# Kernel tuning notes

Measured on AMD Instinct MI355X. Metric: run time of the kernel, lower is better.

The kernel has to match this reference:

```python
import jax, jax.numpy as jnp
import numpy as np

EPS = 1e-5

def _layer_norm(x, gamma, beta):
    # LayerNorm over the last two dims [C, 128], matching nn.LayerNorm([C, 128])
    mean = jnp.mean(x, axis=(-2, -1), keepdims=True)
    var = jnp.var(x, axis=(-2, -1), keepdims=True)
    return (x - mean) * jax.lax.rsqrt(var + EPS) * gamma + beta


def setup_inputs() -> dict:
    key = jax.random.key(0)
    ks = jax.random.split(key, 7)
    B, C, N, L = 64, 1024, 128, 512
    W_SCALE = 0.02  # keep pre-softmax logits / activations in a sane range
    return {
        "X_in": jax.random.normal(ks[0], (B, C, N), jnp.float32),
        "T": jax.random.normal(ks[1], (B, C, L), jnp.float32),
        "Wq": jax.random.normal(ks[2], (C, C), jnp.float32) * W_SCALE,
        "Wk": jax.random.normal(ks[3], (C, C), jnp.float32) * W_SCALE,
        "Wv": jax.random.normal(ks[4], (C, C), jnp.float32) * W_SCALE,
        "Wf1": jax.random.normal(ks[5], (C, C), jnp.float32) * W_SCALE,
        "Wf2": jax.random.normal(ks[6], (C, C), jnp.float32) * W_SCALE,
        "gamma": jnp.ones((C, N), jnp.float32),
        "beta": jnp.zeros((C, N), jnp.float32),
    }


def reference(X_in, T, Wq, Wk, Wv, Wf1, Wf2, gamma, beta):
    C = Wq.shape[1]  # feature_map_cs (intended value of the buggy X_in.weight.shape[1])
    # 1x1 Conv1d == per-position channel matmul: weight [out, in]
    q = jnp.einsum('oc,bcn->bon', Wq, X_in)      # [B, C, N]
    k = jnp.einsum('oc,bcl->bol', Wk, T)         # [B, C, L]
    sim = jnp.einsum('bcn,bcl->bnl', q, k) / jnp.sqrt(jnp.float32(C))  # [B, N, L]
    attn = jax.nn.softmax(sim, axis=2)           # softmax over tokens L
    v = jnp.einsum('oc,bcl->bol', Wv, T)         # [B, C, L]
    ctx = jnp.einsum('bcl,bnl->bcn', v, attn)    # [B, C, N] == bmm(values, attn^T)
    X_out = _layer_norm(X_in + ctx, gamma, beta)
    h = jax.nn.relu(jnp.einsum('oc,bcn->bon', Wf1, X_out))
    ffn = jnp.einsum('oc,bcn->bon', Wf2, h)
    return _layer_norm(X_out + ffn, gamma, beta)
```

## Files before the change

### kernel.cpp

```cpp
#include <hip/hip_runtime.h>


using bf16   = __bf16;
using bf16x4 = __attribute__((ext_vector_type(4))) __bf16;
using bf16x8 = __attribute__((ext_vector_type(8))) __bf16;
using f32x4  = __attribute__((ext_vector_type(4))) float;

static constexpr int  Bb = 64;
static constexpr int  Cc = 1024;
static constexpr int  Nn = 128;
static constexpr int  Ll = 512;
static constexpr long long PLANE = (long long)Cc * Nn;
static constexpr float INV_PLANE = 1.0f / 131072.0f;

__device__ __forceinline__ void gload_lds16(const void* g, void* l) {
    __builtin_amdgcn_global_load_lds(
        (__attribute__((address_space(1))) void*)g,
        (__attribute__((address_space(3))) void*)l,
        16, 0, 0);
}

__global__ void __launch_bounds__(256)
prep_all(const float* __restrict__ Wv, const float* __restrict__ Wf1,
         const float* __restrict__ Wf2, const float* __restrict__ Wq,
         const float* __restrict__ Wk, const float* __restrict__ X,
         bf16* __restrict__ WvB, bf16* __restrict__ Wf1B, bf16* __restrict__ Wf2B,
         bf16* __restrict__ WqT, bf16* __restrict__ WkT, bf16* __restrict__ Xt) {
    __shared__ float tile[64][65];
    const int bx = blockIdx.x;
    const int t  = threadIdx.x;
    if (bx < 3072) {
        const float* in = bx < 1024 ? Wv : (bx < 2048 ? Wf1 : Wf2);
        bf16* out       = bx < 1024 ? WvB : (bx < 2048 ? Wf1B : Wf2B);
        int i = (bx & 1023) * 256 + t;
        float4 v = reinterpret_cast<const float4*>(in)[i];
        bf16x4 o = { (bf16)v.x, (bf16)v.y, (bf16)v.z, (bf16)v.w };
        reinterpret_cast<bf16x4*>(out)[i] = o;
        return;
    }
    const float* in; bf16* outT;
    int R, S, bxx, byy, bz = 0;
    if (bx < 3584) {
        int j = bx - 3072;
        in = (j >= 256) ? Wk : Wq; outT = (j >= 256) ? WkT : WqT;
        R = Cc; S = Cc; j &= 255; bxx = j & 15; byy = j >> 4;
    } else {
        int j = bx - 3584; bz = j >> 5; j &= 31;
        bxx = j & 1; byy = j >> 1; in = X; outT = Xt; R = Cc; S = Nn;
    }
    long long plane = (long long)R * S;
    in   += (long long)bz * plane;
    outT += (long long)bz * plane;
    int s0 = bxx * 64, r0 = byy * 64;
    int rl = t >> 4, sc = (t & 15) * 4;
    #pragma unroll
    for (int p = 0; p < 4; ++p) {
        int r = p * 16 + rl;
        float4 v = *(const float4*)(in + (long long)(r0 + r) * S + s0 + sc);
        *(float4*)&tile[r][sc] = v;
    }
    __syncthreads();
    long long tb = ((long long)(s0 >> 6) * (R >> 6) + (r0 >> 6)) * 4096;
    int sb = t >> 3, rg = (t & 7) * 8;
    #pragma unroll
    for (int p = 0; p < 2; ++p) {
        int s = sb + p * 32;
        bf16x8 o;
        #pragma unroll
        for (int j = 0; j < 8; ++j) o[j] = (bf16)tile[rg + j][s];
        *(bf16x8*)(outT + tb + s * 64 + rg) = o;
    }
}

#define GEMM_PROLOGUE_AND_LOOP(A_, Bt_, KLOOP_, LD_, TA_, TB_)                     \
    __shared__ bf16 As[2][128 * 64];                                               \
    __shared__ bf16 Bs[2][128 * 64];                                               \
    const int n0   = blockIdx.x * 128;                                             \
    const int m0   = blockIdx.y * 128;                                             \
    const int t    = threadIdx.x;                                                  \
    const int lane = t & 63;                                                       \
    const int w    = t >> 6;                                                       \
    const int wr   = (w >> 1) * 64;                                                \
    const int wc   = (w & 1) * 64;                                                 \
    const int lr   = lane & 15;                                                    \
    const int hi4  = (lane >> 4) * 16;                                             \
    const int sw   = (lr & 7) << 4;                                                \
    const int stepA_ = (TA_) ? 4096 : 64;                                          \
    const int stepB_ = (TB_) ? 4096 : 64;                                          \
    const bf16* gA[4]; const bf16* gB[4]; int lo[4];                               \
    _Pragma("unroll")                                                              \
    for (int p = 0; p < 4; ++p) {                                                  \
        int o = w * 1024 + lane * 16 + p * 4096;                                   \
        int row = o >> 7;                                                          \
        int scol = ((o & 127) ^ ((row & 7) << 4)) >> 1;                            \
        lo[p] = o;                                                                 \
        int ra = m0 + row, rb = n0 + row;                                          \
        gA[p] = (TA_) ? A_ + ((long long)(ra >> 6) * (LD_ >> 6)) * 4096            \
                           + (ra & 63) * 64 + scol                                 \
                      : A_ + (long long)ra * LD_ + scol;                           \
        gB[p] = (TB_) ? Bt_ + ((long long)(rb >> 6) * (LD_ >> 6)) * 4096           \
                            + (rb & 63) * 64 + scol                                \
                      : Bt_ + (long long)rb * LD_ + scol;                          \
    }                                                                              \
    f32x4 acc[4][4] = {};                                                          \
    const int NT_ = KLOOP_ / 64;                                                   \
    _Pragma("unroll")                                                              \
    for (int p = 0; p < 4; ++p) gload_lds16(gA[p], (char*)As[0] + lo[p]);          \
    _Pragma("unroll")                                                              \
    for (int p = 0; p < 4; ++p) gload_lds16(gB[p], (char*)Bs[0] + lo[p]);          \
    __syncthreads();                                                               \
    int cur_ = 0;                                                                  \
    for (int kt = 0; kt < NT_; ++kt) {                                             \
        if (kt + 1 < NT_) {                                                        \
            _Pragma("unroll")                                                      \
            for (int p = 0; p < 4; ++p)                                            \
                gload_lds16(gA[p] + (long long)(kt + 1) * stepA_,                  \
                            (char*)As[cur_ ^ 1] + lo[p]);                          \
            _Pragma("unroll")                                                      \
            for (int p = 0; p < 4; ++p)                                            \
                gload_lds16(gB[p] + (long long)(kt + 1) * stepB_,                  \
                            (char*)Bs[cur_ ^ 1] + lo[p]);                          \
        }                                                                          \
        const bf16* As_ = As[cur_]; const bf16* Bs_ = Bs[cur_];                    \
        _Pragma("unroll")                                                          \
        for (int kk = 0; kk < 2; ++kk) {                                           \
            bf16x8 af[4], bfr[4];                                                  \
            _Pragma("unroll")                                                      \
            for (int i = 0; i < 4; ++i) {                                          \
                int ra = wr + i * 16 + lr;                                         \
                int rb = wc + i * 16 + lr;                                         \
                af[i]  = *(const bf16x8*)((const char*)As_ +                       \
                          ((((ra << 7) + (kk << 6) + hi4)) ^ sw));                 \
                bfr[i] = *(const bf16x8*)((const char*)Bs_ +                       \
                          ((((rb << 7) + (kk << 6) + hi4)) ^ sw));                 \
            }                                                                      \
            _Pragma("unroll")                                                      \
            for (int mi = 0; mi < 4; ++mi)                                         \
                _Pragma("unroll")                                                  \
                for (int ni = 0; ni < 4; ++ni)                                     \
                    acc[mi][ni] = __builtin_amdgcn_mfma_f32_16x16x32_bf16(         \
                        af[mi], bfr[ni], acc[mi][ni], 0, 0, 0);                    \
        }                                                                          \
        __syncthreads();                                                           \
        cur_ ^= 1;                                                                 \
    }

template <typename OutT, bool RELU, int TA, int TB>
__global__ void __launch_bounds__(256, 2)
gemm_tn(const bf16* __restrict__ A, const bf16* __restrict__ Bt, OutT* __restrict__ C,
        int M, int N, int KLOOP, int ld, long long sA, long long sBt, long long sC,
        float scale) {
    A  += (long long)blockIdx.z * sA;
    Bt += (long long)blockIdx.z * sBt;
    C  += (long long)blockIdx.z * sC;
    GEMM_PROLOGUE_AND_LOOP(A, Bt, KLOOP, ld, TA, TB)
    const int rbase = m0 + wr + (lane >> 4) * 4;
    const int cbase = n0 + wc + lr;
    #pragma unroll
    for (int mi = 0; mi < 4; ++mi)
        #pragma unroll
        for (int ni = 0; ni < 4; ++ni)
            #pragma unroll
            for (int r = 0; r < 4; ++r) {
                float v = acc[mi][ni][r] * scale;
                if (RELU) v = fmaxf(v, 0.0f);
                C[(long long)(rbase + mi * 16 + r) * N + (cbase + ni * 16)] = (OutT)v;
            }
}

__global__ void g2_reduce(const float* __restrict__ p, bf16* __restrict__ g2) {
    int i = (blockIdx.x * 256 + threadIdx.x) * 4;
    float4 a = *(const float4*)(p + i);
    float4 b = *(const float4*)(p + 1048576 + i);
    float4 c = *(const float4*)(p + 2097152 + i);
    float4 d = *(const float4*)(p + 3145728 + i);
    bf16x4 o = { (bf16)(a.x + b.x + c.x + d.x), (bf16)(a.y + b.y + c.y + d.y),
                 (bf16)(a.z + b.z + c.z + d.z), (bf16)(a.w + b.w + c.w + d.w) };
    *(bf16x4*)(g2 + i) = o;
}

__global__ void __launch_bounds__(256, 3)
gemm_sim_exp(const bf16* __restrict__ A , const float* __restrict__ Tg,
             bf16* __restrict__ E, float* __restrict__ rspart) {
    __shared__ char smem[50432];
    bf16*  Asb = (bf16*)smem;
    bf16*  Bs  = (bf16*)(smem + 16384);
    bf16*  scr = (bf16*)(smem + 32768);
    float* rs  = (float*)(smem + 49408);
    A  += (long long)blockIdx.z * ((long long)Nn * Cc);
    Tg += (long long)blockIdx.z * ((long long)Cc * Ll);
    E  += (long long)blockIdx.z * ((long long)Nn * Ll);
    const int n0 = blockIdx.x * 128;
    const int t = threadIdx.x, lane = t & 63, w = t >> 6;
    const int wr = (w >> 1) * 64, wc = (w & 1) * 64;
    const int lr = lane & 15, hi4 = (lane >> 4) * 16, sw = (lr & 7) << 4;
    const bf16* gA[4]; int lo[4];
    #pragma unroll
    for (int p = 0; p < 4; ++p) {
        int o = w * 1024 + lane * 16 + p * 4096;
        int row = o >> 7;
        int scol = ((o & 127) ^ ((row & 7) << 4)) >> 1;
        lo[p] = o;
        gA[p] = A + (long long)row * Cc + scol;
    }
    const int s1_rc = t >> 2, s1_l = (t & 3) * 32;
    const int s2_l = t & 127, s2_ch = (t >> 7) * 8;
    float4 treg[8];
    #pragma unroll
    for (int i = 0; i < 8; ++i)
        treg[i] = *(const float4*)(Tg + (long long)s1_rc * Ll + n0 + s1_l + i * 4);
    f32x4 acc[4][4] = {};
    const int NT = Cc / 64;
    for (int kt = 0; kt < NT; ++kt) {
        #pragma unroll
        for (int i = 0; i < 8; ++i) {
            float4 v = treg[i];
            bf16x4 o = { (bf16)v.x, (bf16)v.y, (bf16)v.z, (bf16)v.w };
            *(bf16x4*)(scr + s1_rc * 130 + s1_l + i * 4) = o;
        }
        __syncthreads();
        #pragma unroll
        for (int p = 0; p < 4; ++p) gload_lds16(gA[p] + kt * 64, (char*)Asb + lo[p]);
        #pragma unroll
        for (int g = 0; g < 4; ++g) {
            int c0 = s2_ch + g * 16;
            bf16x8 bv;
            #pragma unroll
            for (int j = 0; j < 8; ++j) bv[j] = scr[(c0 + j) * 130 + s2_l];
            *(bf16x8*)((char*)Bs + ((s2_l * 128 + c0 * 2) ^ ((s2_l & 7) << 4))) = bv;
        }
        if (kt + 1 < NT) {
            #pragma unroll
            for (int i = 0; i < 8; ++i)
                treg[i] = *(const float4*)(Tg + (long long)((kt + 1) * 64 + s1_rc) * Ll
                                           + n0 + s1_l + i * 4);
        }
        __syncthreads();
        #pragma unroll
        for (int kk = 0; kk < 2; ++kk) {
            bf16x8 af[4], bfr[4];
            #pragma unroll
            for (int i = 0; i < 4; ++i) {
                int ra = wr + i * 16 + lr;
                int rb = wc + i * 16 + lr;
                af[i]  = *(const bf16x8*)((const char*)Asb + (((ra << 7) + (kk << 6) + hi4) ^ sw));
                bfr[i] = *(const bf16x8*)((const char*)Bs  + (((rb << 7) + (kk << 6) + hi4) ^ sw));
            }
            #pragma unroll
            for (int mi = 0; mi < 4; ++mi)
                #pragma unroll
                for (int ni = 0; ni < 4; ++ni)
                    acc[mi][ni] = __builtin_amdgcn_mfma_f32_16x16x32_bf16(
                        af[mi], bfr[ni], acc[mi][ni], 0, 0, 0);
        }
    }
    const int rbase = wr + (lane >> 4) * 4;
    const int cbase = n0 + wc + lr;
    float psum[4][4];
    #pragma unroll
    for (int mi = 0; mi < 4; ++mi)
        #pragma unroll
        for (int r = 0; r < 4; ++r) psum[mi][r] = 0.f;
    #pragma unroll
    for (int mi = 0; mi < 4; ++mi)
        #pragma unroll
        for (int ni = 0; ni < 4; ++ni)
            #pragma unroll
            for (int r = 0; r < 4; ++r) {
                float ev = __expf(acc[mi][ni][r] * 0.03125f);
                E[(long long)(rbase + mi * 16 + r) * Ll + (cbase + ni * 16)] = (bf16)ev;
                psum[mi][r] += ev;
            }
    #pragma unroll
    for (int mi = 0; mi < 4; ++mi)
        #pragma unroll
        for (int r = 0; r < 4; ++r) {
            float v = psum[mi][r];
            v += __shfl_xor(v, 1); v += __shfl_xor(v, 2);
            v += __shfl_xor(v, 4); v += __shfl_xor(v, 8);
            psum[mi][r] = v;
        }
    __syncthreads();
    if (lr == 0) {
        #pragma unroll
        for (int mi = 0; mi < 4; ++mi)
            #pragma unroll
            for (int r = 0; r < 4; ++r)
                rs[(wc ? 1 : 0) * 128 + wr + (lane >> 4) * 4 + mi * 16 + r] = psum[mi][r];
    }
    __syncthreads();
    if (t < 128)
        rspart[((long long)blockIdx.z * 4 + blockIdx.x) * 128 + t] = rs[t] + rs[128 + t];
}

__global__ void __launch_bounds__(256, 2)
gemm_u_scaled(const bf16* __restrict__ A , const float* __restrict__ Tg,
              bf16* __restrict__ C, const float* __restrict__ rspart) {
    __shared__ char smem[49152];
    bf16* AsB = (bf16*)smem;
    bf16* Bs  = (bf16*)(smem + 32768);
    A  += (long long)blockIdx.z * ((long long)Nn * Ll);
    Tg += (long long)blockIdx.z * ((long long)Cc * Ll);
    C  += (long long)blockIdx.z * ((long long)Nn * Cc);
    const float* rp = rspart + (long long)blockIdx.z * 512;
    const int n0 = blockIdx.x * 128;
    const int t = threadIdx.x, lane = t & 63, w = t >> 6;
    const int wr = (w >> 1) * 64, wc = (w & 1) * 64;
    const int lr = lane & 15, hi4 = (lane >> 4) * 16, sw = (lr & 7) << 4;
    const bf16* gA[4]; int lo[4];
    #pragma unroll
    for (int p = 0; p < 4; ++p) {
        int o = w * 1024 + lane * 16 + p * 4096;
        int row = o >> 7;
        int scol = ((o & 127) ^ ((row & 7) << 4)) >> 1;
        lo[p] = o;
        gA[p] = A + (long long)row * Ll + scol;
    }
    const int s_c = t >> 1, s_half = (t & 1) * 32;
    float4 treg[8];
    #pragma unroll
    for (int p = 0; p < 4; ++p) gload_lds16(gA[p], (char*)AsB + lo[p]);
    #pragma unroll
    for (int i = 0; i < 8; ++i)
        treg[i] = *(const float4*)(Tg + (long long)(n0 + s_c) * Ll + s_half + i * 4);
    f32x4 acc[4][4] = {};
    int cur = 0;
    const int NT = Ll / 64;
    for (int kt = 0; kt < NT; ++kt) {
        if (kt + 1 < NT) {
            #pragma unroll
            for (int p = 0; p < 4; ++p)
                gload_lds16(gA[p] + (kt + 1) * 64, (char*)AsB + (cur ^ 1) * 16384 + lo[p]);
        }
        __syncthreads();
        #pragma unroll
        for (int q = 0; q < 4; ++q) {
            bf16x8 bv;
            #pragma unroll
            for (int j = 0; j < 4; ++j) {
                bv[j]     = (bf16)((const float*)&treg[q * 2])[j];
                bv[4 + j] = (bf16)((const float*)&treg[q * 2 + 1])[j];
            }
            *(bf16x8*)((char*)Bs + ((s_c * 128 + (s_half + q * 8) * 2) ^ ((s_c & 7) << 4))) = bv;
        }
        if (kt + 1 < NT) {
            #pragma unroll
            for (int i = 0; i < 8; ++i)
                treg[i] = *(const float4*)(Tg + (long long)(n0 + s_c) * Ll
                                           + (kt + 1) * 64 + s_half + i * 4);
        }
        __syncthreads();
        const bf16* As_ = AsB + cur * 8192;
        #pragma unroll
        for (int kk = 0; kk < 2; ++kk) {
            bf16x8 af[4], bfr[4];
            #pragma unroll
            for (int i = 0; i < 4; ++i) {
                int ra = wr + i * 16 + lr;
                int rb = wc + i * 16 + lr;
                af[i]  = *(const bf16x8*)((const char*)As_ + (((ra << 7) + (kk << 6) + hi4) ^ sw));
                bfr[i] = *(const bf16x8*)((const char*)Bs  + (((rb << 7) + (kk << 6) + hi4) ^ sw));
            }
            #pragma unroll
            for (int mi = 0; mi < 4; ++mi)
                #pragma unroll
                for (int ni = 0; ni < 4; ++ni)
                    acc[mi][ni] = __builtin_amdgcn_mfma_f32_16x16x32_bf16(
                        af[mi], bfr[ni], acc[mi][ni], 0, 0, 0);
        }
        cur ^= 1;
    }
    const int rbase = wr + (lane >> 4) * 4;
    const int cbase = n0 + wc + lr;
    #pragma unroll
    for (int mi = 0; mi < 4; ++mi)
        #pragma unroll
        for (int r = 0; r < 4; ++r) {
            int row = rbase + mi * 16 + r;
            float inv = 1.f / (rp[row] + rp[128 + row] + rp[256 + row] + rp[384 + row]);
            #pragma unroll
            for (int ni = 0; ni < 4; ++ni)
                C[(long long)row * Cc + (cbase + ni * 16)] = (bf16)(acc[mi][ni][r] * inv);
        }
}

__global__ void __launch_bounds__(256, 2)
gemm_ctx_ln1(const bf16* __restrict__ A , const bf16* __restrict__ Bt ,
             const float* __restrict__ X, bf16* __restrict__ Z1, float* __restrict__ partials,
             int K, long long sBt) {
    const int N = Nn;
    Bt += (long long)blockIdx.z * sBt;
    X  += (long long)blockIdx.z * PLANE;
    Z1 += (long long)blockIdx.z * PLANE;
    GEMM_PROLOGUE_AND_LOOP(A, Bt, K, K, 0, 0)
    const int rbase = m0 + wr + (lane >> 4) * 4;
    const int cbase = n0 + wc + lr;
    float s = 0.f, ss = 0.f;
    #pragma unroll
    for (int mi = 0; mi < 4; ++mi)
        #pragma unroll
        for (int ni = 0; ni < 4; ++ni)
            #pragma unroll
            for (int r = 0; r < 4; ++r) {
                long long idx = (long long)(rbase + mi * 16 + r) * N + (cbase + ni * 16);
                float zv = acc[mi][ni][r] + X[idx];
                Z1[idx] = (bf16)zv;
                s += zv; ss += zv * zv;
            }
    #pragma unroll
    for (int off = 32; off; off >>= 1) { s += __shfl_xor(s, off); ss += __shfl_xor(ss, off); }
    __shared__ float red[8];
    if (lane == 0) { red[w] = s; red[4 + w] = ss; }
    __syncthreads();
    if (t == 0) {
        float S = red[0] + red[1] + red[2] + red[3];
        float SS = red[4] + red[5] + red[6] + red[7];
        float* p = partials + ((long long)blockIdx.z * 8 + blockIdx.y) * 2;
        p[0] = S; p[1] = SS;
    }
}

__global__ void __launch_bounds__(256, 2)
gemm_ffn_ln2(const bf16* __restrict__ A , const bf16* __restrict__ Bt ,
             const bf16* __restrict__ Z1, const float* __restrict__ pp1,
             const float* __restrict__ gamma, const float* __restrict__ beta,
             bf16* __restrict__ Z2, float* __restrict__ partials,
             int K, long long sA) {
    A  += (long long)blockIdx.z * sA;
    Z1 += (long long)blockIdx.z * PLANE;
    Z2 += (long long)blockIdx.z * PLANE;
    float S1 = 0.f, SS1 = 0.f;
    #pragma unroll
    for (int j = 0; j < 8; ++j) {
        S1  += pp1[((long long)blockIdx.z * 8 + j) * 2];
        SS1 += pp1[((long long)blockIdx.z * 8 + j) * 2 + 1];
    }
    const float mean1 = S1 * INV_PLANE;
    const float rstd1 = rsqrtf(SS1 * INV_PLANE - mean1 * mean1 + 1e-5f);
    GEMM_PROLOGUE_AND_LOOP(A, Bt, K, K, 0, 0)
    const int rbase = m0 + wr + (lane >> 4) * 4;
    const int cbase = n0 + wc + lr;
    float s = 0.f, ss = 0.f;
    #pragma unroll
    for (int mi = 0; mi < 4; ++mi)
        #pragma unroll
        for (int ni = 0; ni < 4; ++ni) {
            long long a = (long long)(cbase + ni * 16) * Nn + rbase + mi * 16;
            bf16x4 z1v = *(const bf16x4*)(Z1 + a);
            float4 g  = *(const float4*)(gamma + a);
            float4 be = *(const float4*)(beta + a);
            float x0 = ((float)z1v[0] - mean1) * rstd1 * g.x + be.x;
            float x1 = ((float)z1v[1] - mean1) * rstd1 * g.y + be.y;
            float x2 = ((float)z1v[2] - mean1) * rstd1 * g.z + be.z;
            float x3 = ((float)z1v[3] - mean1) * rstd1 * g.w + be.w;
            float z0 = acc[mi][ni][0] + x0, z1 = acc[mi][ni][1] + x1;
            float z2 = acc[mi][ni][2] + x2, z3 = acc[mi][ni][3] + x3;
            bf16x4 zo = { (bf16)z0, (bf16)z1, (bf16)z2, (bf16)z3 };
            *(bf16x4*)(Z2 + a) = zo;
            s  += z0 + z1 + z2 + z3;
            ss += z0 * z0 + z1 * z1 + z2 * z2 + z3 * z3;
        }
    #pragma unroll
    for (int off = 32; off; off >>= 1) { s += __shfl_xor(s, off); ss += __shfl_xor(ss, off); }
    __shared__ float red[8];
    if (lane == 0) { red[w] = s; red[4 + w] = ss; }
    __syncthreads();
    if (t == 0) {
        float S = red[0] + red[1] + red[2] + red[3];
        float SS = red[4] + red[5] + red[6] + red[7];
        float* p = partials + ((long long)blockIdx.z * 8 + blockIdx.x) * 2;
        p[0] = S; p[1] = SS;
    }
}

__global__ void ln1_norm_transpose(const bf16* __restrict__ Z1, const float* __restrict__ partials,
                                   const float* __restrict__ gamma, const float* __restrict__ beta,
                                   bf16* __restrict__ XoutT) {
    int b = blockIdx.z;
    float S = 0.f, SS = 0.f;
    #pragma unroll
    for (int j = 0; j < 8; ++j) {
        S  += partials[((long long)b * 8 + j) * 2];
        SS += partials[((long long)b * 8 + j) * 2 + 1];
    }
    float mean = S * INV_PLANE;
    float rstd = rsqrtf(SS * INV_PLANE - mean * mean + 1e-5f);
    __shared__ float tile[64][65];
    long long base = (long long)b * PLANE;
    int n0 = blockIdx.x * 64, c0 = blockIdx.y * 64;
    int t = threadIdx.x;
    int rl = t >> 4, sc = (t & 15) * 4;
    #pragma unroll
    for (int p = 0; p < 4; ++p) {
        int r = p * 16 + rl;
        long long idx = (long long)(c0 + r) * Nn + n0 + sc;
        bf16x4 z  = *(const bf16x4*)(Z1 + base + idx);
        float4 g  = *(const float4*)(gamma + idx);
        float4 be = *(const float4*)(beta + idx);
        float4 o = {((float)z[0] - mean) * rstd * g.x + be.x,
                    ((float)z[1] - mean) * rstd * g.y + be.y,
                    ((float)z[2] - mean) * rstd * g.z + be.z,
                    ((float)z[3] - mean) * rstd * g.w + be.w};
        *(float4*)&tile[r][sc] = o;
    }
    __syncthreads();
    long long tb = ((long long)(n0 >> 6) * (Cc >> 6) + (c0 >> 6)) * 4096;
    int sb = t >> 3, rg = (t & 7) * 8;
    #pragma unroll
    for (int p = 0; p < 2; ++p) {
        int n = sb + p * 32;
        bf16x8 o;
        #pragma unroll
        for (int j = 0; j < 8; ++j) o[j] = (bf16)tile[rg + j][n];
        *(bf16x8*)(XoutT + base + tb + n * 64 + rg) = o;
    }
}

__global__ void ln2_final(const bf16* __restrict__ Z2, const float* __restrict__ partials,
                          const float* __restrict__ gamma, const float* __restrict__ beta,
                          float* __restrict__ out) {
    int b = blockIdx.y;
    float S = 0.f, SS = 0.f;
    #pragma unroll
    for (int j = 0; j < 8; ++j) {
        S  += partials[((long long)b * 8 + j) * 2];
        SS += partials[((long long)b * 8 + j) * 2 + 1];
    }
    float mean = S * INV_PLANE;
    float rstd = rsqrtf(SS * INV_PLANE - mean * mean + 1e-5f);
    long long base = (long long)b * PLANE;
    int i = (blockIdx.x * 256 + threadIdx.x) * 8;
    bf16x8 z = *(const bf16x8*)(Z2 + base + i);
    #pragma unroll
    for (int h = 0; h < 2; ++h) {
        float4 g  = *(const float4*)(gamma + i + h * 4);
        float4 be = *(const float4*)(beta + i + h * 4);
        float4 o = {((float)z[h * 4 + 0] - mean) * rstd * g.x + be.x,
                    ((float)z[h * 4 + 1] - mean) * rstd * g.y + be.y,
                    ((float)z[h * 4 + 2] - mean) * rstd * g.z + be.z,
                    ((float)z[h * 4 + 3] - mean) * rstd * g.w + be.w};
        *(float4*)(out + base + i + h * 4) = o;
    }
}

extern "C" void kernel_launch(void* const* d_in, const int* in_sizes, int n_in,
                              void* d_out, int out_size, void* d_ws, size_t ws_size,
                              hipStream_t stream) {
    const float* X   = (const float*)d_in[0];
    const float* T   = (const float*)d_in[1];
    const float* Wq  = (const float*)d_in[2];
    const float* Wk  = (const float*)d_in[3];
    const float* Wv  = (const float*)d_in[4];
    const float* Wf1 = (const float*)d_in[5];
    const float* Wf2 = (const float*)d_in[6];
    const float* gamma = (const float*)d_in[7];
    const float* beta  = (const float*)d_in[8];
    float* out = (float*)d_out;
    char* ws = (char*)d_ws;
    const size_t MB = 1ull << 20;

    bf16* WvB  = (bf16*)(ws + 0 * MB);
    bf16* Wf1B = (bf16*)(ws + 2 * MB);
    bf16* Wf2B = (bf16*)(ws + 4 * MB);
    bf16* WqT  = (bf16*)(ws + 6 * MB);
    bf16* WkT  = (bf16*)(ws + 8 * MB);
    bf16* G2   = (bf16*)(ws + 10 * MB);
    bf16* Xt   = (bf16*)(ws + 12 * MB);
    bf16* Z1   = (bf16*)(ws + 28 * MB);
    bf16* XoutT= (bf16*)(ws + 44 * MB);
    bf16* hT   = (bf16*)(ws + 60 * MB);
    bf16* e    = (bf16*)(ws + 76 * MB);
    bf16* Z2   = (bf16*)(ws + 92 * MB);
    bf16* E    = (bf16*)(ws + 108 * MB);
    bf16* u    = (bf16*)(ws + 116 * MB);
    float* G2p = (float*)(ws + 132 * MB);
    float* pp1 = (float*)(ws + 148 * MB);
    float* pp2 = (float*)(ws + 148 * MB + 65536);
    float* rsp = (float*)(ws + 149 * MB);

    dim3 blk256(256);

    prep_all<<<dim3(5632), blk256, 0, stream>>>(
        Wv, Wf1, Wf2, Wq, Wk, X, WvB, Wf1B, Wf2B, WqT, WkT, Xt);

    gemm_tn<float, false, 1, 1><<<dim3(8, 8, 4), blk256, 0, stream>>>(
        WkT, WqT, G2p, Cc, Cc, 256, Cc, 16384, 16384, 1048576, 1.f);
    g2_reduce<<<dim3(1024), blk256, 0, stream>>>(G2p, G2);

    gemm_tn<bf16, false, 1, 0><<<dim3(8, 1, Bb), blk256, 0, stream>>>(
        Xt, G2, e, Nn, Cc, Cc, Cc, (long long)Nn * Cc, 0, (long long)Nn * Cc, 1.f);
    gemm_sim_exp<<<dim3(4, 1, Bb), blk256, 0, stream>>>(e, T, E, rsp);
    gemm_u_scaled<<<dim3(8, 1, Bb), blk256, 0, stream>>>(E, T, u, rsp);
    gemm_ctx_ln1<<<dim3(1, 8, Bb), blk256, 0, stream>>>(
        WvB, u, X, Z1, pp1, Cc, (long long)Nn * Cc);
    ln1_norm_transpose<<<dim3(Nn / 64, Cc / 64, Bb), blk256, 0, stream>>>(
        Z1, pp1, gamma, beta, XoutT);
    gemm_tn<bf16, true, 1, 0><<<dim3(8, 1, Bb), blk256, 0, stream>>>(
        XoutT, Wf1B, hT, Nn, Cc, Cc, Cc, (long long)Nn * Cc, 0, (long long)Nn * Cc, 1.f);
    gemm_ffn_ln2<<<dim3(8, 1, Bb), blk256, 0, stream>>>(
        hT, Wf2B, Z1, pp1, gamma, beta, Z2, pp2, Cc, (long long)Nn * Cc);
    ln2_final<<<dim3(64, Bb), blk256, 0, stream>>>(Z2, pp2, gamma, beta, out);
}
```

Baseline: 279.8 us.

## Halve N-tile width in sim-exp and u-scaled GEMMs to double block count

Both attention GEMMs now tile 128x64 instead of 128x128, so each block has 4 warps each covering 32 rows by 64 columns, and the grid doubles to 512 and 1024 blocks. The row-sum partials grow from 4 to 8 per batch and are written directly without the LDS reduction, and the consumer sums 8 partials. Smaller tiles raise parallelism and occupancy (smaller LDS, fewer accumulators) but each block re-reads the full A operand, doubling A traffic and lowering MFMA reuse per LDS load.

After: 258.0 us (median of 2 runs). 7.8% less time.

```diff
diff --git a/kernel.cpp b/kernel.cpp
--- a/kernel.cpp
+++ b/kernel.cpp
@@ -179,20 +179,18 @@
     *(bf16x4*)(g2 + i) = o;
 }
 
-__global__ void __launch_bounds__(256, 3)
+__global__ void __launch_bounds__(256, 2)
 gemm_sim_exp(const bf16* __restrict__ A , const float* __restrict__ Tg,
              bf16* __restrict__ E, float* __restrict__ rspart) {
-    __shared__ char smem[50432];
-    bf16*  Asb = (bf16*)smem;
-    bf16*  Bs  = (bf16*)(smem + 16384);
-    bf16*  scr = (bf16*)(smem + 32768);
-    float* rs  = (float*)(smem + 49408);
+    __shared__ char smem[33024];
+    bf16* Asb = (bf16*)smem;
+    bf16* Bs  = (bf16*)(smem + 16384);
+    bf16* scr = (bf16*)(smem + 24576);
     A  += (long long)blockIdx.z * ((long long)Nn * Cc);
     Tg += (long long)blockIdx.z * ((long long)Cc * Ll);
     E  += (long long)blockIdx.z * ((long long)Nn * Ll);
-    const int n0 = blockIdx.x * 128;
+    const int l0 = blockIdx.x * 64;
     const int t = threadIdx.x, lane = t & 63, w = t >> 6;
-    const int wr = (w >> 1) * 64, wc = (w & 1) * 64;
     const int lr = lane & 15, hi4 = (lane >> 4) * 16, sw = (lr & 7) << 4;
     const bf16* gA[4]; int lo[4];
     #pragma unroll
@@ -203,76 +201,80 @@
         lo[p] = o;
         gA[p] = A + (long long)row * Cc + scol;
     }
-    const int s1_rc = t >> 2, s1_l = (t & 3) * 32;
-    const int s2_l = t & 127, s2_ch = (t >> 7) * 8;
-    float4 treg[8];
-    #pragma unroll
-    for (int i = 0; i < 8; ++i)
-        treg[i] = *(const float4*)(Tg + (long long)s1_rc * Ll + n0 + s1_l + i * 4);
-    f32x4 acc[4][4] = {};
+    const int s_c = t >> 2, s_l = (t & 3) * 16;
+    float4 treg[4];
+    #pragma unroll
+    for (int i = 0; i < 4; ++i)
+        treg[i] = *(const float4*)(Tg + (long long)s_c * Ll + l0 + s_l + i * 4);
+    f32x4 acc[2][4] = {};
     const int NT = Cc / 64;
     for (int kt = 0; kt < NT; ++kt) {
         #pragma unroll
-        for (int i = 0; i < 8; ++i) {
+        for (int i = 0; i < 4; ++i) {
             float4 v = treg[i];
             bf16x4 o = { (bf16)v.x, (bf16)v.y, (bf16)v.z, (bf16)v.w };
-            *(bf16x4*)(scr + s1_rc * 130 + s1_l + i * 4) = o;
+            *(bf16x4*)(scr + s_c * 66 + s_l + i * 4) = o;
         }
         __syncthreads();
         #pragma unroll
         for (int p = 0; p < 4; ++p) gload_lds16(gA[p] + kt * 64, (char*)Asb + lo[p]);
-        #pragma unroll
-        for (int g = 0; g < 4; ++g) {
-            int c0 = s2_ch + g * 16;
-            bf16x8 bv;
-            #pragma unroll
-            for (int j = 0; j < 8; ++j) bv[j] = scr[(c0 + j) * 130 + s2_l];
-            *(bf16x8*)((char*)Bs + ((s2_l * 128 + c0 * 2) ^ ((s2_l & 7) << 4))) = bv;
+        {
+            int lrow = t & 63;
+            #pragma unroll
+            for (int p = 0; p < 2; ++p) {
+                int c8 = (t >> 6) * 16 + p * 8;
+                bf16x8 bv;
+                #pragma unroll
+                for (int j = 0; j < 8; ++j) bv[j] = scr[(c8 + j) * 66 + lrow];
+                *(bf16x8*)((char*)Bs + (((lrow << 7) + c8 * 2) ^ ((lrow & 7) << 4))) = bv;
+            }
         }
         if (kt + 1 < NT) {
             #pragma unroll
-            for (int i = 0; i < 8; ++i)
-                treg[i] = *(const float4*)(Tg + (long long)((kt + 1) * 64 + s1_rc) * Ll
-                                           + n0 + s1_l + i * 4);
+            for (int i = 0; i < 4; ++i)
+                treg[i] = *(const float4*)(Tg + (long long)((kt + 1) * 64 + s_c) * Ll
+                                           + l0 + s_l + i * 4);
         }
         __syncthreads();
         #pragma unroll
         for (int kk = 0; kk < 2; ++kk) {
-            bf16x8 af[4], bfr[4];
-            #pragma unroll
-            for (int i = 0; i < 4; ++i) {
-                int ra = wr + i * 16 + lr;
-                int rb = wc + i * 16 + lr;
-                af[i]  = *(const bf16x8*)((const char*)Asb + (((ra << 7) + (kk << 6) + hi4) ^ sw));
-                bfr[i] = *(const bf16x8*)((const char*)Bs  + (((rb << 7) + (kk << 6) + hi4) ^ sw));
-            }
-            #pragma unroll
-            for (int mi = 0; mi < 4; ++mi)
+            bf16x8 af[2], bfr[4];
+            #pragma unroll
+            for (int mi = 0; mi < 2; ++mi) {
+                int ra = w * 32 + mi * 16 + lr;
+                af[mi] = *(const bf16x8*)((const char*)Asb + (((ra << 7) + (kk << 6) + hi4) ^ sw));
+            }
+            #pragma unroll
+            for (int ni = 0; ni < 4; ++ni) {
+                int rb = ni * 16 + lr;
+                bfr[ni] = *(const bf16x8*)((const char*)Bs + (((rb << 7) + (kk << 6) + hi4) ^ sw));
+            }
+            #pragma unroll
+            for (int mi = 0; mi < 2; ++mi)
                 #pragma unroll
                 for (int ni = 0; ni < 4; ++ni)
                     acc[mi][ni] = __builtin_amdgcn_mfma_f32_16x16x32_bf16(
                         af[mi], bfr[ni], acc[mi][ni], 0, 0, 0);
         }
     }
-    const int rbase = wr + (lane >> 4) * 4;
-    const int cbase = n0 + wc + lr;
-    float psum[4][4];
-    #pragma unroll
-    for (int mi = 0; mi < 4; ++mi)
+    float psum[2][4];
+    #pragma unroll
+    for (int mi = 0; mi < 2; ++mi)
         #pragma unroll
         for (int r = 0; r < 4; ++r) psum[mi][r] = 0.f;
     #pragma unroll
-    for (int mi = 0; mi < 4; ++mi)
+    for (int mi = 0; mi < 2; ++mi)
         #pragma unroll
         for (int ni = 0; ni < 4; ++ni)
             #pragma unroll
             for (int r = 0; r < 4; ++r) {
+                int row = w * 32 + mi * 16 + (lane >> 4) * 4 + r;
                 float ev = __expf(acc[mi][ni][r] * 0.03125f);
-                E[(long long)(rbase + mi * 16 + r) * Ll + (cbase + ni * 16)] = (bf16)ev;
+                E[(long long)row * Ll + l0 + ni * 16 + lr] = (bf16)ev;
                 psum[mi][r] += ev;
             }
     #pragma unroll
-    for (int mi = 0; mi < 4; ++mi)
+    for (int mi = 0; mi < 2; ++mi)
         #pragma unroll
         for (int r = 0; r < 4; ++r) {
             float v = psum[mi][r];
@@ -280,32 +282,28 @@
             v += __shfl_xor(v, 4); v += __shfl_xor(v, 8);
             psum[mi][r] = v;
         }
-    __syncthreads();
     if (lr == 0) {
-        #pragma unroll
-        for (int mi = 0; mi < 4; ++mi)
+        float* rp = rspart + ((long long)blockIdx.z * 8 + blockIdx.x) * 128;
+        #pragma unroll
+        for (int mi = 0; mi < 2; ++mi)
             #pragma unroll
             for (int r = 0; r < 4; ++r)
-                rs[(wc ? 1 : 0) * 128 + wr + (lane >> 4) * 4 + mi * 16 + r] = psum[mi][r];
-    }
-    __syncthreads();
-    if (t < 128)
-        rspart[((long long)blockIdx.z * 4 + blockIdx.x) * 128 + t] = rs[t] + rs[128 + t];
-}
-
-__global__ void __launch_bounds__(256, 2)
+                rp[w * 32 + mi * 16 + (lane >> 4) * 4 + r] = psum[mi][r];
+    }
+}
+
+__global__ void __launch_bounds__(256, 4)
 gemm_u_scaled(const bf16* __restrict__ A , const float* __restrict__ Tg,
               bf16* __restrict__ C, const float* __restrict__ rspart) {
-    __shared__ char smem[49152];
+    __shared__ char smem[40960];
     bf16* AsB = (bf16*)smem;
     bf16* Bs  = (bf16*)(smem + 32768);
     A  += (long long)blockIdx.z * ((long long)Nn * Ll);
     Tg += (long long)blockIdx.z * ((long long)Cc * Ll);
     C  += (long long)blockIdx.z * ((long long)Nn * Cc);
-    const float* rp = rspart + (long long)blockIdx.z * 512;
-    const int n0 = blockIdx.x * 128;
+    const float* rp = rspart + (long long)blockIdx.z * 1024;
+    const int c0 = blockIdx.x * 64;
     const int t = threadIdx.x, lane = t & 63, w = t >> 6;
-    const int wr = (w >> 1) * 64, wc = (w & 1) * 64;
     const int lr = lane & 15, hi4 = (lane >> 4) * 16, sw = (lr & 7) << 4;
     const bf16* gA[4]; int lo[4];
     #pragma unroll
@@ -316,14 +314,14 @@
         lo[p] = o;
         gA[p] = A + (long long)row * Ll + scol;
     }
-    const int s_c = t >> 1, s_half = (t & 1) * 32;
-    float4 treg[8];
+    const int s_c = t >> 2, s_l = (t & 3) * 16;
+    float4 treg[4];
     #pragma unroll
     for (int p = 0; p < 4; ++p) gload_lds16(gA[p], (char*)AsB + lo[p]);
     #pragma unroll
-    for (int i = 0; i < 8; ++i)
-        treg[i] = *(const float4*)(Tg + (long long)(n0 + s_c) * Ll + s_half + i * 4);
-    f32x4 acc[4][4] = {};
+    for (int i = 0; i < 4; ++i)
+        treg[i] = *(const float4*)(Tg + (long long)(c0 + s_c) * Ll + s_l + i * 4);
+    f32x4 acc[2][4] = {};
     int cur = 0;
     const int NT = Ll / 64;
     for (int kt = 0; kt < NT; ++kt) {
@@ -334,35 +332,38 @@
         }
         __syncthreads();
         #pragma unroll
-        for (int q = 0; q < 4; ++q) {
+        for (int p = 0; p < 2; ++p) {
             bf16x8 bv;
             #pragma unroll
             for (int j = 0; j < 4; ++j) {
-                bv[j]     = (bf16)((const float*)&treg[q * 2])[j];
-                bv[4 + j] = (bf16)((const float*)&treg[q * 2 + 1])[j];
-            }
-            *(bf16x8*)((char*)Bs + ((s_c * 128 + (s_half + q * 8) * 2) ^ ((s_c & 7) << 4))) = bv;
+                bv[j]     = (bf16)((const float*)&treg[p * 2])[j];
+                bv[4 + j] = (bf16)((const float*)&treg[p * 2 + 1])[j];
+            }
+            *(bf16x8*)((char*)Bs + (((s_c << 7) + (s_l + p * 8) * 2) ^ ((s_c & 7) << 4))) = bv;
         }
         if (kt + 1 < NT) {
             #pragma unroll
-            for (int i = 0; i < 8; ++i)
-                treg[i] = *(const float4*)(Tg + (long long)(n0 + s_c) * Ll
-                                           + (kt + 1) * 64 + s_half + i * 4);
+            for (int i = 0; i < 4; ++i)
+                treg[i] = *(const float4*)(Tg + (long long)(c0 + s_c) * Ll
+                                           + (kt + 1) * 64 + s_l + i * 4);
         }
         __syncthreads();
         const bf16* As_ = AsB + cur * 8192;
         #pragma unroll
         for (int kk = 0; kk < 2; ++kk) {
-            bf16x8 af[4], bfr[4];
-            #pragma unroll
-            for (int i = 0; i < 4; ++i) {
-                int ra = wr + i * 16 + lr;
-                int rb = wc + i * 16 + lr;
-                af[i]  = *(const bf16x8*)((const char*)As_ + (((ra << 7) + (kk << 6) + hi4) ^ sw));
-                bfr[i] = *(const bf16x8*)((const char*)Bs  + (((rb << 7) + (kk << 6) + hi4) ^ sw));
-            }
-            #pragma unroll
-            for (int mi = 0; mi < 4; ++mi)
+            bf16x8 af[2], bfr[4];
+            #pragma unroll
+            for (int mi = 0; mi < 2; ++mi) {
+                int ra = w * 32 + mi * 16 + lr;
+                af[mi] = *(const bf16x8*)((const char*)As_ + (((ra << 7) + (kk << 6) + hi4) ^ sw));
+            }
+            #pragma unroll
+            for (int ni = 0; ni < 4; ++ni) {
+                int rb = ni * 16 + lr;
+                bfr[ni] = *(const bf16x8*)((const char*)Bs + (((rb << 7) + (kk << 6) + hi4) ^ sw));
+            }
+            #pragma unroll
+            for (int mi = 0; mi < 2; ++mi)
                 #pragma unroll
                 for (int ni = 0; ni < 4; ++ni)
                     acc[mi][ni] = __builtin_amdgcn_mfma_f32_16x16x32_bf16(
@@ -370,17 +371,18 @@
         }
         cur ^= 1;
     }
-    const int rbase = wr + (lane >> 4) * 4;
-    const int cbase = n0 + wc + lr;
-    #pragma unroll
-    for (int mi = 0; mi < 4; ++mi)
+    #pragma unroll
+    for (int mi = 0; mi < 2; ++mi)
         #pragma unroll
         for (int r = 0; r < 4; ++r) {
-            int row = rbase + mi * 16 + r;
-            float inv = 1.f / (rp[row] + rp[128 + row] + rp[256 + row] + rp[384 + row]);
+            int row = w * 32 + mi * 16 + (lane >> 4) * 4 + r;
+            float s = 0.f;
+            #pragma unroll
+            for (int j = 0; j < 8; ++j) s += rp[j * 128 + row];
+            float inv = 1.f / s;
             #pragma unroll
             for (int ni = 0; ni < 4; ++ni)
-                C[(long long)row * Cc + (cbase + ni * 16)] = (bf16)(acc[mi][ni][r] * inv);
+                C[(long long)row * Cc + (c0 + ni * 16 + lr)] = (bf16)(acc[mi][ni][r] * inv);
         }
 }
 
@@ -589,8 +591,8 @@
 
     gemm_tn<bf16, false, 1, 0><<<dim3(8, 1, Bb), blk256, 0, stream>>>(
         Xt, G2, e, Nn, Cc, Cc, Cc, (long long)Nn * Cc, 0, (long long)Nn * Cc, 1.f);
-    gemm_sim_exp<<<dim3(4, 1, Bb), blk256, 0, stream>>>(e, T, E, rsp);
-    gemm_u_scaled<<<dim3(8, 1, Bb), blk256, 0, stream>>>(E, T, u, rsp);
+    gemm_sim_exp<<<dim3(8, 1, Bb), blk256, 0, stream>>>(e, T, E, rsp);
+    gemm_u_scaled<<<dim3(16, 1, Bb), blk256, 0, stream>>>(E, T, u, rsp);
     gemm_ctx_ln1<<<dim3(1, 8, Bb), blk256, 0, stream>>>(
         WvB, u, X, Z1, pp1, Cc, (long long)Nn * Cc);
     ln1_norm_transpose<<<dim3(Nn / 64, Cc / 64, Bb), blk256, 0, stream>>>(
```
